# Kernel tuning notes

Hardware: AMD Instinct MI355X
Metric: run time of the kernel (lower is better)

## Reference

```python
import jax, jax.numpy as jnp
import numpy as np

NUM_NEURONS = 256
NUM_SAMPLES = 512
MAX_SPIKES = 32
N_STEPS = 32          # fixed RK4 steps per spike round (stands in for adaptive Tsit5)
ALPHA = 0.03
V_RESET = 1.0
T0 = 0.0


def setup_inputs() -> dict:
    key = jax.random.key(0)
    ks = jax.random.split(key, 7)
    input_current = jax.random.normal(ks[0], (NUM_NEURONS,), dtype=jnp.float32)
    # _build_w with network=all-False: uniform(minval=0.5), mask sets nothing
    w = jax.random.uniform(ks[1], (NUM_NEURONS, NUM_NEURONS), minval=0.5, maxval=1.0, dtype=jnp.float32)
    mu = jax.random.uniform(ks[2], (2,), minval=0.5, maxval=1.0, dtype=jnp.float32)
    v0 = jax.random.normal(ks[3], (NUM_NEURONS,), dtype=jnp.float32)
    i0 = jax.random.normal(ks[4], (NUM_NEURONS,), dtype=jnp.float32)
    # s0 = log(U) - alpha  (always < 0)
    s0 = (jnp.log(jax.random.uniform(ks[5], (NUM_SAMPLES, NUM_NEURONS), minval=1e-6, maxval=1.0)) - ALPHA).astype(jnp.float32)
    # pre-drawn stochastic resets, one per (spike round, sample, neuron)
    reset_s = (jnp.log(jax.random.uniform(ks[6], (MAX_SPIKES, NUM_SAMPLES, NUM_NEURONS), minval=1e-6, maxval=1.0)) - ALPHA).astype(jnp.float32)
    return dict(input_current=input_current, w=w, mu=mu, v0=v0, i0=i0, s0=s0, reset_s=reset_s, t1=2)


def _drift(y, ic, mu1, mu2):
    # y: [samples, neurons, 3] = (v, i, s)
    v, i = y[..., 0], y[..., 1]
    dv = mu1 * (i + ic - v)
    di = -mu2 * i
    ds = jax.nn.sigmoid(v)  # intensity_fn(v)
    return jnp.stack([dv, di, ds], axis=-1)


def reference(input_current, w, mu, v0, i0, s0, reset_s, t1):
    t1f = jnp.float32(t1)
    mu1, mu2 = mu[0], mu[1]
    ic = input_current  # constant-in-time input current, [neurons]

    y0 = jnp.concatenate([
        jnp.broadcast_to(v0, (NUM_SAMPLES, NUM_NEURONS))[..., None],
        jnp.broadcast_to(i0, (NUM_SAMPLES, NUM_NEURONS))[..., None],
        s0[..., None]], axis=-1)  # [samples, neurons, 3]

    def rk4(y, h):
        k1 = _drift(y, ic, mu1, mu2)
        k2 = _drift(y + 0.5 * h * k1, ic, mu1, mu2)
        k3 = _drift(y + 0.5 * h * k2, ic, mu1, mu2)
        k4 = _drift(y + h * k3, ic, mu1, mu2)
        return y + (h / 6.0) * (k1 + 2.0 * k2 + 2.0 * k3 + k4)

    def round_body(carry, reset_k):
        t0s, y_in = carry                      # t0s: [samples]
        dt = (t1f - t0s) / N_STEPS             # per-sample step size
        h = dt[:, None, None]

        def step(sc, _):
            t, y, done, tev, yev, emask = sc
            y_new = rk4(y, h)
            y_new = jnp.where(done[:, None, None], y, y_new)  # freeze after event
            s_prev, s_new = y[..., 2], y_new[..., 2]
            crossed = s_new > 0.0                              # cond_fn root: s crosses 0
            trig = crossed.any(axis=1) & (~done)
            idx = jnp.argmax(s_new, axis=1)                    # event neuron (first/largest crossing)
            sp = jnp.take_along_axis(s_prev, idx[:, None], 1)[:, 0]
            sn = jnp.take_along_axis(s_new, idx[:, None], 1)[:, 0]
            frac = jnp.clip(sp / (sp - sn + 1e-12), 0.0, 1.0)  # linear root estimate (Newton stand-in)
            t_c = t + frac * dt
            y_c = y + frac[:, None, None] * (y_new - y)
            tev = jnp.where(trig, t_c, tev)
            yev = jnp.where(trig[:, None, None], y_c, yev)
            emask = jnp.where(trig[:, None], crossed, emask)
            y = jnp.where(trig[:, None, None], y_c, y_new)
            done = done | trig
            return (t + dt, y, done, tev, yev, emask), None

        done0 = jnp.zeros((NUM_SAMPLES,), bool)
        tev0 = jnp.full((NUM_SAMPLES,), jnp.inf, jnp.float32)
        em0 = jnp.zeros((NUM_SAMPLES, NUM_NEURONS), bool)
        (_, yend, done, tev, yev, emask), _ = jax.lax.scan(
            step, (t0s, y_in, done0, tev0, y_in, em0), None, length=N_STEPS)

        tev = jnp.where(done, tev, t1f)                 # no event -> sol.ts[-1] = t1
        yev = jnp.where(done[:, None, None], yev, yend)

        # trans_fn: spike reset + synaptic jump w[event_idx]
        eidx = jnp.argmax(emask, axis=1)
        w_row = jnp.where(done[:, None], w[eidx], 0.0)  # zero if no event happened
        v_t = yev[..., 0] - jnp.where(emask, V_RESET, 0.0)
        i_t = yev[..., 1] + w_row
        s_t = jnp.minimum(jnp.where(emask, reset_k, yev[..., 2]), 0.0)
        y_next = jnp.stack([v_t, i_t, s_t], axis=-1)
        return (tev, y_next), (tev, yev, emask)

    t0s = jnp.full((NUM_SAMPLES,), T0, jnp.float32)
    _, (tevs, yevs, emasks) = jax.lax.scan(jax.checkpoint(round_body), (t0s, y0), reset_s)

    spike_times = jnp.transpose(tevs, (1, 0))            # [samples, max_spikes]
    spike_values = jnp.transpose(yevs, (1, 0, 2, 3))     # [samples, max_spikes, neurons, 3]
    spike_marks = jnp.transpose(emasks, (1, 0, 2))       # [samples, max_spikes, neurons]
    return spike_times, spike_values, spike_marks
```

## Files before the change

kernel.cpp:

```cpp
#include <hip/hip_runtime.h>
#include <math.h>

#define NN 256
#define NS 512
#define MS 32
#define NSTEP 32
#define VRESET 1.0f

__device__ __forceinline__ float sigf(float x) {
    float e = __expf(-x);
    return __builtin_amdgcn_rcpf(1.0f + e);
}

__global__ __launch_bounds__(64) void snn_kernel(
    const float* __restrict__ ic_g,
    const float* __restrict__ w,
    const float* __restrict__ mu,
    const float* __restrict__ v0,
    const float* __restrict__ i0,
    const float* __restrict__ s0,
    const float* __restrict__ reset_s,
    const int*   __restrict__ t1p,
    float* __restrict__ out)
{
    const int lane = threadIdx.x;
    const int samp = blockIdx.x;
    const float mu1 = mu[0];
    const float mu2 = mu[1];
    const float t1f = (float)t1p[0];

    float v[4], ii[4], s[4], ic[4];
#pragma unroll
    for (int j = 0; j < 4; ++j) {
        int n = lane + 64 * j;
        v[j]  = v0[n];
        ii[j] = i0[n];
        s[j]  = s0[samp * NN + n];
        ic[j] = ic_g[n];
    }
    float t0 = 0.0f;

    float* times = out;
    float* vals  = out + (size_t)NS * MS;
    float* marks = out + (size_t)NS * MS * (1 + NN * 3);

    for (int r = 0; r < MS; ++r) {
        const float dt = (t1f - t0) / (float)NSTEP;
        float tev = t1f;
        float yev_v[4], yev_i[4], yev_s[4];
        bool  em[4];
        bool  done = false;

        if (dt != 0.0f) {
            float t = t0;
            const float hh = 0.5f * dt;
            const float h6 = dt * (1.0f / 6.0f);
            for (int st = 0; st < NSTEP; ++st) {
                float vn[4], inw[4], sn[4];
#pragma unroll
                for (int j = 0; j < 4; ++j) {
                    float kv1 = mu1 * (ii[j] + ic[j] - v[j]);
                    float ki1 = -mu2 * ii[j];
                    float ks1 = sigf(v[j]);
                    float v2 = v[j] + hh * kv1;
                    float i2 = ii[j] + hh * ki1;
                    float kv2 = mu1 * (i2 + ic[j] - v2);
                    float ki2 = -mu2 * i2;
                    float ks2 = sigf(v2);
                    float v3 = v[j] + hh * kv2;
                    float i3 = ii[j] + hh * ki2;
                    float kv3 = mu1 * (i3 + ic[j] - v3);
                    float ki3 = -mu2 * i3;
                    float ks3 = sigf(v3);
                    float v4 = v[j] + dt * kv3;
                    float i4 = ii[j] + dt * ki3;
                    float kv4 = mu1 * (i4 + ic[j] - v4);
                    float ki4 = -mu2 * i4;
                    float ks4 = sigf(v4);
                    vn[j]  = v[j]  + h6 * (kv1 + 2.0f * kv2 + 2.0f * kv3 + kv4);
                    inw[j] = ii[j] + h6 * (ki1 + 2.0f * ki2 + 2.0f * ki3 + ki4);
                    sn[j]  = s[j]  + h6 * (ks1 + 2.0f * ks2 + 2.0f * ks3 + ks4);
                }
                bool any4 = (sn[0] > 0.0f) | (sn[1] > 0.0f) |
                            (sn[2] > 0.0f) | (sn[3] > 0.0f);
                if (__any(any4)) {
                    float bv = sn[0], bsp = s[0];
                    int   bn = lane;
#pragma unroll
                    for (int j = 1; j < 4; ++j) {
                        if (sn[j] > bv) { bv = sn[j]; bsp = s[j]; bn = lane + 64 * j; }
                    }
#pragma unroll
                    for (int off = 32; off >= 1; off >>= 1) {
                        float ov  = __shfl_xor(bv, off);
                        float osp = __shfl_xor(bsp, off);
                        int   on  = __shfl_xor(bn, off);
                        if (ov > bv || (ov == bv && on < bn)) { bv = ov; bsp = osp; bn = on; }
                    }
                    float frac = bsp / (bsp - bv + 1e-12f);
                    frac = fminf(fmaxf(frac, 0.0f), 1.0f);
                    tev = t + frac * dt;
#pragma unroll
                    for (int j = 0; j < 4; ++j) {
                        yev_v[j] = v[j]  + frac * (vn[j]  - v[j]);
                        yev_i[j] = ii[j] + frac * (inw[j] - ii[j]);
                        yev_s[j] = s[j]  + frac * (sn[j]  - s[j]);
                        em[j] = sn[j] > 0.0f;
                        v[j] = yev_v[j]; ii[j] = yev_i[j]; s[j] = yev_s[j];
                    }
                    done = true;
                    break;
                }
#pragma unroll
                for (int j = 0; j < 4; ++j) { v[j] = vn[j]; ii[j] = inw[j]; s[j] = sn[j]; }
                t += dt;
            }
        }

        if (!done) {
            tev = t1f;
#pragma unroll
            for (int j = 0; j < 4; ++j) {
                yev_v[j] = v[j]; yev_i[j] = ii[j]; yev_s[j] = s[j]; em[j] = false;
            }
        }

        const int sr = samp * MS + r;
        if (lane == 0) times[sr] = tev;
#pragma unroll
        for (int j = 0; j < 4; ++j) {
            int n = lane + 64 * j;
            float* p = vals + ((size_t)sr * NN + n) * 3;
            p[0] = yev_v[j];
            p[1] = yev_i[j];
            p[2] = yev_s[j];
            marks[(size_t)sr * NN + n] = em[j] ? 1.0f : 0.0f;
        }

        if (done) {
            int cand = 2 * NN;
#pragma unroll
            for (int j = 3; j >= 0; --j) if (em[j]) cand = lane + 64 * j;
#pragma unroll
            for (int off = 32; off >= 1; off >>= 1) {
                int oc = __shfl_xor(cand, off);
                cand = (oc < cand) ? oc : cand;
            }
            const int eidx = cand;
#pragma unroll
            for (int j = 0; j < 4; ++j) {
                int n = lane + 64 * j;
                float wr = w[eidx * NN + n];
                v[j]  = yev_v[j] - (em[j] ? VRESET : 0.0f);
                ii[j] = yev_i[j] + wr;
                float sres = em[j] ? reset_s[((size_t)r * NS + samp) * NN + n] : yev_s[j];
                s[j] = fminf(sres, 0.0f);
            }
        } else {
#pragma unroll
            for (int j = 0; j < 4; ++j) s[j] = fminf(s[j], 0.0f);
        }
        t0 = tev;
    }
}

extern "C" void kernel_launch(void* const* d_in, const int* in_sizes, int n_in,
                              void* d_out, int out_size, void* d_ws, size_t ws_size,
                              hipStream_t stream) {
    const float* ic      = (const float*)d_in[0];
    const float* w       = (const float*)d_in[1];
    const float* mu      = (const float*)d_in[2];
    const float* v0      = (const float*)d_in[3];
    const float* i0      = (const float*)d_in[4];
    const float* s0      = (const float*)d_in[5];
    const float* reset_s = (const float*)d_in[6];
    const int*   t1p     = (const int*)d_in[7];
    float* out = (float*)d_out;

    snn_kernel<<<dim3(NS), dim3(64), 0, stream>>>(ic, w, mu, v0, i0, s0,
                                                  reset_s, t1p, out);
}
```

Baseline: 153.9 us.

## Spread each sample's neurons across four wavefronts with shared-memory reductions

Each block now runs 256 threads, one neuron per thread, instead of one 64-lane wavefront handling four neurons per lane. The per-step any-spike test, argmax and event-index search become cross-wave reductions through shared memory with __syncthreads. The aim is to expose more parallelism and cut the serial RK4 dependency chain per thread on a GPU where 512 single-wave blocks underfill the CUs. In exchange it adds a block barrier on every RK4 step.

After: 153.0 us. About the same (-0.6%).

```diff
diff --git a/kernel.cpp b/kernel.cpp
--- a/kernel.cpp
+++ b/kernel.cpp
@@ -12,7 +12,7 @@
     return __builtin_amdgcn_rcpf(1.0f + e);
 }
 
-__global__ __launch_bounds__(64) void snn_kernel(
+__global__ __launch_bounds__(256) void snn_kernel(
     const float* __restrict__ ic_g,
     const float* __restrict__ w,
     const float* __restrict__ mu,
@@ -23,21 +23,23 @@
     const int*   __restrict__ t1p,
     float* __restrict__ out)
 {
-    const int lane = threadIdx.x;
+    const int tid  = threadIdx.x;
+    const int lane = tid & 63;
+    const int wid  = tid >> 6;
     const int samp = blockIdx.x;
     const float mu1 = mu[0];
     const float mu2 = mu[1];
     const float t1f = (float)t1p[0];
 
-    float v[4], ii[4], s[4], ic[4];
-#pragma unroll
-    for (int j = 0; j < 4; ++j) {
-        int n = lane + 64 * j;
-        v[j]  = v0[n];
-        ii[j] = i0[n];
-        s[j]  = s0[samp * NN + n];
-        ic[j] = ic_g[n];
-    }
+    __shared__ int   s_any[2][4];
+    __shared__ float s_bv[4], s_bsp[4];
+    __shared__ int   s_bn[4];
+    __shared__ int   s_eidx[4];
+
+    float v  = v0[tid];
+    float ii = i0[tid];
+    float s  = s0[samp * NN + tid];
+    const float ic = ic_g[tid];
     float t0 = 0.0f;
 
     float* times = out;
@@ -47,8 +49,8 @@
     for (int r = 0; r < MS; ++r) {
         const float dt = (t1f - t0) / (float)NSTEP;
         float tev = t1f;
-        float yev_v[4], yev_i[4], yev_s[4];
-        bool  em[4];
+        float yev_v, yev_i, yev_s;
+        bool  em = false;
         bool  done = false;
 
         if (dt != 0.0f) {
@@ -56,40 +58,37 @@
             const float hh = 0.5f * dt;
             const float h6 = dt * (1.0f / 6.0f);
             for (int st = 0; st < NSTEP; ++st) {
-                float vn[4], inw[4], sn[4];
-#pragma unroll
-                for (int j = 0; j < 4; ++j) {
-                    float kv1 = mu1 * (ii[j] + ic[j] - v[j]);
-                    float ki1 = -mu2 * ii[j];
-                    float ks1 = sigf(v[j]);
-                    float v2 = v[j] + hh * kv1;
-                    float i2 = ii[j] + hh * ki1;
-                    float kv2 = mu1 * (i2 + ic[j] - v2);
-                    float ki2 = -mu2 * i2;
-                    float ks2 = sigf(v2);
-                    float v3 = v[j] + hh * kv2;
-                    float i3 = ii[j] + hh * ki2;
-                    float kv3 = mu1 * (i3 + ic[j] - v3);
-                    float ki3 = -mu2 * i3;
-                    float ks3 = sigf(v3);
-                    float v4 = v[j] + dt * kv3;
-                    float i4 = ii[j] + dt * ki3;
-                    float kv4 = mu1 * (i4 + ic[j] - v4);
-                    float ki4 = -mu2 * i4;
-                    float ks4 = sigf(v4);
-                    vn[j]  = v[j]  + h6 * (kv1 + 2.0f * kv2 + 2.0f * kv3 + kv4);
-                    inw[j] = ii[j] + h6 * (ki1 + 2.0f * ki2 + 2.0f * ki3 + ki4);
-                    sn[j]  = s[j]  + h6 * (ks1 + 2.0f * ks2 + 2.0f * ks3 + ks4);
-                }
-                bool any4 = (sn[0] > 0.0f) | (sn[1] > 0.0f) |
-                            (sn[2] > 0.0f) | (sn[3] > 0.0f);
-                if (__any(any4)) {
-                    float bv = sn[0], bsp = s[0];
-                    int   bn = lane;
-#pragma unroll
-                    for (int j = 1; j < 4; ++j) {
-                        if (sn[j] > bv) { bv = sn[j]; bsp = s[j]; bn = lane + 64 * j; }
-                    }
+                float kv1 = mu1 * (ii + ic - v);
+                float ki1 = -mu2 * ii;
+                float ks1 = sigf(v);
+                float v2 = v + hh * kv1;
+                float i2 = ii + hh * ki1;
+                float kv2 = mu1 * (i2 + ic - v2);
+                float ki2 = -mu2 * i2;
+                float ks2 = sigf(v2);
+                float v3 = v + hh * kv2;
+                float i3 = ii + hh * ki2;
+                float kv3 = mu1 * (i3 + ic - v3);
+                float ki3 = -mu2 * i3;
+                float ks3 = sigf(v3);
+                float v4 = v + dt * kv3;
+                float i4 = ii + dt * ki3;
+                float kv4 = mu1 * (i4 + ic - v4);
+                float ki4 = -mu2 * i4;
+                float ks4 = sigf(v4);
+                float vn = v  + h6 * (kv1 + 2.0f * kv2 + 2.0f * kv3 + kv4);
+                float in_ = ii + h6 * (ki1 + 2.0f * ki2 + 2.0f * ki3 + ki4);
+                float sn = s  + h6 * (ks1 + 2.0f * ks2 + 2.0f * ks3 + ks4);
+
+                unsigned long long bl = __ballot(sn > 0.0f);
+                if (lane == 0) s_any[st & 1][wid] = (bl != 0ull) ? 1 : 0;
+                __syncthreads();
+                int anyflag = s_any[st & 1][0] | s_any[st & 1][1] |
+                              s_any[st & 1][2] | s_any[st & 1][3];
+
+                if (anyflag) {
+                    float bv = sn, bsp = s;
+                    int   bn = tid;
 #pragma unroll
                     for (int off = 32; off >= 1; off >>= 1) {
                         float ov  = __shfl_xor(bv, off);
@@ -97,68 +96,63 @@
                         int   on  = __shfl_xor(bn, off);
                         if (ov > bv || (ov == bv && on < bn)) { bv = ov; bsp = osp; bn = on; }
                     }
+                    if (lane == 0) { s_bv[wid] = bv; s_bsp[wid] = bsp; s_bn[wid] = bn; }
+                    __syncthreads();
+                    bv = s_bv[0]; bsp = s_bsp[0]; bn = s_bn[0];
+#pragma unroll
+                    for (int wv = 1; wv < 4; ++wv) {
+                        float ov = s_bv[wv], osp = s_bsp[wv];
+                        int   on = s_bn[wv];
+                        if (ov > bv || (ov == bv && on < bn)) { bv = ov; bsp = osp; bn = on; }
+                    }
                     float frac = bsp / (bsp - bv + 1e-12f);
                     frac = fminf(fmaxf(frac, 0.0f), 1.0f);
                     tev = t + frac * dt;
-#pragma unroll
-                    for (int j = 0; j < 4; ++j) {
-                        yev_v[j] = v[j]  + frac * (vn[j]  - v[j]);
-                        yev_i[j] = ii[j] + frac * (inw[j] - ii[j]);
-                        yev_s[j] = s[j]  + frac * (sn[j]  - s[j]);
-                        em[j] = sn[j] > 0.0f;
-                        v[j] = yev_v[j]; ii[j] = yev_i[j]; s[j] = yev_s[j];
-                    }
+                    yev_v = v  + frac * (vn - v);
+                    yev_i = ii + frac * (in_ - ii);
+                    yev_s = s  + frac * (sn - s);
+                    em = sn > 0.0f;
+                    v = yev_v; ii = yev_i; s = yev_s;
                     done = true;
                     break;
                 }
-#pragma unroll
-                for (int j = 0; j < 4; ++j) { v[j] = vn[j]; ii[j] = inw[j]; s[j] = sn[j]; }
+                v = vn; ii = in_; s = sn;
                 t += dt;
             }
         }
 
         if (!done) {
             tev = t1f;
-#pragma unroll
-            for (int j = 0; j < 4; ++j) {
-                yev_v[j] = v[j]; yev_i[j] = ii[j]; yev_s[j] = s[j]; em[j] = false;
-            }
+            yev_v = v; yev_i = ii; yev_s = s; em = false;
         }
 
         const int sr = samp * MS + r;
-        if (lane == 0) times[sr] = tev;
-#pragma unroll
-        for (int j = 0; j < 4; ++j) {
-            int n = lane + 64 * j;
-            float* p = vals + ((size_t)sr * NN + n) * 3;
-            p[0] = yev_v[j];
-            p[1] = yev_i[j];
-            p[2] = yev_s[j];
-            marks[(size_t)sr * NN + n] = em[j] ? 1.0f : 0.0f;
+        if (tid == 0) times[sr] = tev;
+        {
+            float* p = vals + ((size_t)sr * NN + tid) * 3;
+            p[0] = yev_v;
+            p[1] = yev_i;
+            p[2] = yev_s;
+            marks[(size_t)sr * NN + tid] = em ? 1.0f : 0.0f;
         }
 
         if (done) {
-            int cand = 2 * NN;
-#pragma unroll
-            for (int j = 3; j >= 0; --j) if (em[j]) cand = lane + 64 * j;
-#pragma unroll
-            for (int off = 32; off >= 1; off >>= 1) {
-                int oc = __shfl_xor(cand, off);
-                cand = (oc < cand) ? oc : cand;
-            }
-            const int eidx = cand;
-#pragma unroll
-            for (int j = 0; j < 4; ++j) {
-                int n = lane + 64 * j;
-                float wr = w[eidx * NN + n];
-                v[j]  = yev_v[j] - (em[j] ? VRESET : 0.0f);
-                ii[j] = yev_i[j] + wr;
-                float sres = em[j] ? reset_s[((size_t)r * NS + samp) * NN + n] : yev_s[j];
-                s[j] = fminf(sres, 0.0f);
-            }
+            unsigned long long bm = __ballot(em);
+            int cand = (bm != 0ull) ? (wid * 64 + (int)__builtin_ctzll(bm)) : (2 * NN);
+            if (lane == 0) s_eidx[wid] = cand;
+            __syncthreads();
+            int eidx = s_eidx[0];
+            eidx = (s_eidx[1] < eidx) ? s_eidx[1] : eidx;
+            eidx = (s_eidx[2] < eidx) ? s_eidx[2] : eidx;
+            eidx = (s_eidx[3] < eidx) ? s_eidx[3] : eidx;
+
+            float wr = w[eidx * NN + tid];
+            v  = yev_v - (em ? VRESET : 0.0f);
+            ii = yev_i + wr;
+            float sres = em ? reset_s[((size_t)r * NS + samp) * NN + tid] : yev_s;
+            s = fminf(sres, 0.0f);
         } else {
-#pragma unroll
-            for (int j = 0; j < 4; ++j) s[j] = fminf(s[j], 0.0f);
+            s = fminf(s, 0.0f);
         }
         t0 = tev;
     }
@@ -177,6 +171,6 @@
     const int*   t1p     = (const int*)d_in[7];
     float* out = (float*)d_out;
 
-    snn_kernel<<<dim3(NS), dim3(64), 0, stream>>>(ic, w, mu, v0, i0, s0,
-                                                  reset_s, t1p, out);
+    snn_kernel<<<dim3(NS), dim3(256), 0, stream>>>(ic, w, mu, v0, i0, s0,
+                                                   reset_s, t1p, out);
 }
```
